# Kernel optimization log

Measured on AMD Instinct MI355X. Metric: run time of the kernel, lower is better.

Reference implementation:

```python
import jax, jax.numpy as jnp
import numpy as np

N_NODES = 50000


def _relgraphconv(x, W, Wloop, b, src, dst, etypes, n_nodes):
    # DGL RelGraphConv (regularizer=None, self_loop=True, norm=None):
    # out[i] = sum over incoming edges (j->i, rel r) of W_r @ x[j]  +  W_loop @ x[i]  +  b
    # low-mem form: transform all nodes per relation, then gather per edge.
    h_rel = jnp.einsum('ni,rio->rno', x, W)          # [R, N, out]
    msg = h_rel[etypes, src]                          # [E, out]
    agg = jax.ops.segment_sum(msg, dst, num_segments=n_nodes)  # [N, out]
    return agg + x @ Wloop + b


def setup_inputs() -> dict:
    key = jax.random.key(0)
    ks = jax.random.split(key, 12)
    N, E, n_state = N_NODES, 800000, 128
    inp = {
        'x': jax.random.normal(ks[0], (N, n_state), dtype=jnp.float32),
        'src': jax.random.randint(ks[1], (E,), 0, N, dtype=jnp.int32),
        'dst': jax.random.randint(ks[2], (E,), 0, N, dtype=jnp.int32),
        'etypes': jax.random.randint(ks[3], (E,), 0, 2, dtype=jnp.int32),
        'cell_size': jax.random.randint(ks[4], (N,), 0, 8, dtype=jnp.int32),
        'max_size': jax.random.randint(ks[5], (N,), 0, 8, dtype=jnp.int32),
        'W1': jax.random.normal(ks[6], (2, n_state, 64), dtype=jnp.float32) * 0.05,
        'loop1': jax.random.normal(ks[7], (n_state, 64), dtype=jnp.float32) * 0.05,
        'b1': jnp.zeros((64,), dtype=jnp.float32),
        'W2': jax.random.normal(ks[8], (2, 64, 64), dtype=jnp.float32) * 0.05,
        'loop2': jax.random.normal(ks[9], (64, 64), dtype=jnp.float32) * 0.05,
        'b2': jnp.zeros((64,), dtype=jnp.float32),
        'W3': jax.random.normal(ks[10], (2, 64, 2), dtype=jnp.float32) * 0.05,
        'loop3': jax.random.normal(ks[11], (64, 2), dtype=jnp.float32) * 0.05,
        'b3': jnp.zeros((2,), dtype=jnp.float32),
    }
    return inp


def reference(x, src, dst, etypes, cell_size, max_size,
              W1, loop1, b1, W2, loop2, b2, W3, loop3, b3):
    N = x.shape[0]
    h = jax.nn.relu(_relgraphconv(x, W1, loop1, b1, src, dst, etypes, N))
    h = jax.nn.relu(_relgraphconv(h, W2, loop2, b2, src, dst, etypes, N))
    h = _relgraphconv(h, W3, loop3, b3, src, dst, etypes, N)   # [N, 2]
    # action mask: col 0 = cannot upsize, col 1 = cannot downsize
    upper = cell_size >= (max_size - 1)
    lower = cell_size == 0
    mask = jnp.stack([upper, lower], axis=1)                   # [N, 2] bool
    return jnp.where(mask, h.min() - 1.0, h)
```

## Files before the change

kernel.cpp:

```cpp
#include <hip/hip_runtime.h>


#define STRIDE 64
#define BINCAP 2560

typedef unsigned short ushortT;
typedef __attribute__((ext_vector_type(8))) short short8;
typedef __attribute__((ext_vector_type(4))) float f32x4;

__device__ inline ushortT f2bf(float f) {
    union { float f; unsigned u; } v; v.f = f;
    unsigned r = v.u + 0x7FFFu + ((v.u >> 16) & 1u);
    return (ushortT)(r >> 16);
}
__device__ inline float bf2f(ushortT h) {
    union { unsigned u; float f; } v; v.u = ((unsigned)h) << 16;
    return v.f;
}

__device__ inline void atomicMinF(float* addr, float v) {
    if (v >= 0.f) atomicMin((int*)addr, __float_as_int(v));
    else          atomicMax((unsigned int*)addr, __float_as_uint(v));
}

__global__ __launch_bounds__(256) void pack_init_kernel(
    const float* __restrict__ W1, const float* __restrict__ loop1,
    const float* __restrict__ W2, const float* __restrict__ loop2,
    ushortT* __restrict__ BP1, ushortT* __restrict__ BP2,
    int* __restrict__ bincnt, float* __restrict__ minval, int NBINS) {
    int g = (int)blockIdx.x * 256 + (int)threadIdx.x;
    if (g < NBINS) bincnt[g] = 0;
    if (g == 0) *(int*)minval = 0x7f7f7f7f;
    if (g < 3072) {
        int l = g & 63, ks = (g >> 6) & 3, ct = g >> 8;
        int c = ct * 16 + (l & 15);
        int mat = c >> 6, cc = c & 63;
        int kbase = ks * 32 + (l >> 4) * 8;
        ushortT* dstp = BP1 + (size_t)g * 8;
#pragma unroll
        for (int j = 0; j < 8; ++j) {
            int k = kbase + j;
            float v = (mat < 2) ? W1[((size_t)mat * 128 + k) * 64 + cc]
                                : loop1[(size_t)k * 64 + cc];
            dstp[j] = f2bf(v);
        }
    } else {
        int s = g - 3072;
        int l = s & 63, ks = (s >> 6) & 1, ct = s >> 7;
        int c = ct * 16 + (l & 15);
        int mat = c >> 6, cc = c & 63;
        int kbase = ks * 32 + (l >> 4) * 8;
        ushortT* dstp = BP2 + (size_t)s * 8;
#pragma unroll
        for (int j = 0; j < 8; ++j) {
            int k = kbase + j;
            float v = (mat < 2) ? W2[((size_t)mat * 64 + k) * 64 + cc]
                                : loop2[(size_t)k * 64 + cc];
            dstp[j] = f2bf(v);
        }
    }
}

__global__ __launch_bounds__(256) void k1_kernel(
    const float* __restrict__ x, const ushortT* __restrict__ BP1,
    const float* __restrict__ b1,
    ushortT* __restrict__ hrelb, ushortT* __restrict__ H1b,
    const int* __restrict__ src, const int* __restrict__ dst,
    const int* __restrict__ et, int* __restrict__ bincnt, int2* __restrict__ binbuf,
    int N, int E, int NBINS, int NBA) {
    __shared__ int hist[512];
    __shared__ int gbase[512];
    __shared__ ushortT rnk[4096];

    const int t = (int)threadIdx.x;

    if ((int)blockIdx.x < NBA) {
        for (int i = t; i < NBINS; i += 256) hist[i] = 0;
        __syncthreads();
        const int base = (int)blockIdx.x * 4096;
#pragma unroll
        for (int i = 0; i < 16; ++i) {
            int e = base + t + i * 256;
            if (e < E) {
                int bb = dst[e] >> 7;
                rnk[t + i * 256] = (ushortT)atomicAdd(&hist[bb], 1);
            }
        }
        __syncthreads();
        for (int i = t; i < NBINS; i += 256) {
            int h = hist[i];
            gbase[i] = h ? atomicAdd(&bincnt[i], h) : 0;
        }
        __syncthreads();
#pragma unroll
        for (int i = 0; i < 16; ++i) {
            int e = base + t + i * 256;
            if (e < E) {
                int dd = dst[e];
                int bb = dd >> 7;
                int v = et[e] * N + src[e];
                int pos = gbase[bb] + (int)rnk[t + i * 256];
                if (pos < BINCAP)
                    binbuf[(size_t)bb * BINCAP + pos] = make_int2(dd, v);
            }
        }
        return;
    }
    const int w = t >> 6, lane = t & 63;
    const int rowbase = (((int)blockIdx.x - NBA) * 4 + w) * 16;
    const int m = lane & 15, quad = lane >> 4;
    const int nclamp = min(rowbase + m, N - 1);

    short8 a[4];
    const float* xp = x + (size_t)nclamp * 128 + quad * 8;
#pragma unroll
    for (int ks = 0; ks < 4; ++ks) {
        float4 g0 = *(const float4*)(xp + ks * 32);
        float4 g1 = *(const float4*)(xp + ks * 32 + 4);
        a[ks][0] = (short)f2bf(g0.x); a[ks][1] = (short)f2bf(g0.y);
        a[ks][2] = (short)f2bf(g0.z); a[ks][3] = (short)f2bf(g0.w);
        a[ks][4] = (short)f2bf(g1.x); a[ks][5] = (short)f2bf(g1.y);
        a[ks][6] = (short)f2bf(g1.z); a[ks][7] = (short)f2bf(g1.w);
    }

    f32x4 acc[12];
#pragma unroll
    for (int ct = 0; ct < 12; ++ct) acc[ct] = (f32x4){0.f, 0.f, 0.f, 0.f};

#pragma unroll
    for (int ks = 0; ks < 4; ++ks) {
#pragma unroll
        for (int ct = 0; ct < 12; ++ct) {
            short8 b = *(const short8*)&BP1[((size_t)(ct * 4 + ks) * 64 + lane) * 8];
            acc[ct] = __builtin_amdgcn_mfma_f32_16x16x32_bf16(a[ks], b, acc[ct], 0, 0, 0);
        }
    }

    const int node0 = rowbase + quad * 4;
#pragma unroll
    for (int ct = 0; ct < 12; ++ct) {
        int c = ct * 16 + m;
        int mat = c >> 6, cc = c & 63;
        float bias = (mat == 2) ? b1[cc] : 0.f;
#pragma unroll
        for (int j = 0; j < 4; ++j) {
            int n = node0 + j;
            if (n < N) {
                float v = acc[ct][j] + bias;
                if (mat < 2) hrelb[((size_t)mat * N + n) * 64 + cc] = f2bf(v);
                else         H1b[(size_t)n * 64 + cc] = f2bf(v);
            }
        }
    }
}

__global__ __launch_bounds__(256) void phaseB_kernel(
    const int* __restrict__ bincnt, const int2* __restrict__ binbuf,
    int* __restrict__ cnt, int* __restrict__ eidx, int N) {
    __shared__ int lcnt[128];
    const int b = (int)blockIdx.x;
    const int t = (int)threadIdx.x;
    if (t < 128) lcnt[t] = 0;
    __syncthreads();
    const int cb = min(bincnt[b], BINCAP);
    const int2* buf = binbuf + (size_t)b * BINCAP;
    for (int i = t; i < cb; i += 256) {
        int2 rec = buf[i];
        int r = atomicAdd(&lcnt[rec.x & 127], 1);
        if (r < STRIDE) eidx[(size_t)rec.x * STRIDE + r] = rec.y;
    }
    __syncthreads();
    int node = b * 128 + t;
    if (t < 128 && node < N) cnt[node] = min(lcnt[t], STRIDE);
}

__device__ __forceinline__ float gather_accum(
    const ushortT* __restrict__ hb, int my, int deg, int lane, float acc) {
    for (int j = 0; j < deg; j += 16) {
        float v[16];
#pragma unroll
        for (int q = 0; q < 16; ++q) {
            int jj = j + q;
            int sel = (jj < deg) ? jj : 0;
            int id = __shfl(my, sel, 64);
            float wgt = (jj < deg) ? 1.f : 0.f;
            v[q] = wgt * bf2f(hb[(size_t)id * 64 + lane]);
        }
        float s0 = (v[0] + v[1]) + (v[2] + v[3]);
        float s1 = (v[4] + v[5]) + (v[6] + v[7]);
        float s2 = (v[8] + v[9]) + (v[10] + v[11]);
        float s3 = (v[12] + v[13]) + (v[14] + v[15]);
        acc += (s0 + s1) + (s2 + s3);
    }
    return acc;
}

__global__ void agg1_kernel(const ushortT* __restrict__ hrelb, const int* __restrict__ eidx,
                            const int* __restrict__ cnt, ushortT* __restrict__ H1b, int N) {
    int node = (int)blockIdx.x * 4 + ((int)threadIdx.x >> 6);
    if (node >= N) return;
    int lane = (int)threadIdx.x & 63;
    int deg = cnt[node];
    int my = (lane < deg) ? eidx[(size_t)node * STRIDE + lane] : 0;
    float acc = bf2f(H1b[(size_t)node * 64 + lane]);
    acc = gather_accum(hrelb, my, deg, lane, acc);
    H1b[(size_t)node * 64 + lane] = f2bf(fmaxf(acc, 0.f));
}

__global__ __launch_bounds__(256) void gemm2_mfma(
    const ushortT* __restrict__ H1b, const ushortT* __restrict__ BP2,
    const float* __restrict__ b2,
    ushortT* __restrict__ hrel2b, ushortT* __restrict__ H2b, int N) {
    const int w = (int)threadIdx.x >> 6, lane = (int)threadIdx.x & 63;
    const int rowbase = ((int)blockIdx.x * 4 + w) * 16;
    const int m = lane & 15, quad = lane >> 4;
    const int nclamp = min(rowbase + m, N - 1);

    short8 a[2];
    const ushortT* hp = H1b + (size_t)nclamp * 64 + quad * 8;
    a[0] = *(const short8*)(hp);
    a[1] = *(const short8*)(hp + 32);

    f32x4 acc[12];
#pragma unroll
    for (int ct = 0; ct < 12; ++ct) acc[ct] = (f32x4){0.f, 0.f, 0.f, 0.f};

#pragma unroll
    for (int ks = 0; ks < 2; ++ks) {
#pragma unroll
        for (int ct = 0; ct < 12; ++ct) {
            short8 b = *(const short8*)&BP2[((size_t)(ct * 2 + ks) * 64 + lane) * 8];
            acc[ct] = __builtin_amdgcn_mfma_f32_16x16x32_bf16(a[ks], b, acc[ct], 0, 0, 0);
        }
    }

    const int node0 = rowbase + quad * 4;
#pragma unroll
    for (int ct = 0; ct < 12; ++ct) {
        int c = ct * 16 + m;
        int mat = c >> 6, cc = c & 63;
        float bias = (mat == 2) ? b2[cc] : 0.f;
#pragma unroll
        for (int j = 0; j < 4; ++j) {
            int n = node0 + j;
            if (n < N) {
                float v = acc[ct][j] + bias;
                if (mat < 2) hrel2b[((size_t)mat * N + n) * 64 + cc] = f2bf(v);
                else         H2b[(size_t)n * 64 + cc] = f2bf(v);
            }
        }
    }
}

__global__ void k3_kernel(const ushortT* __restrict__ hrel2b, const ushortT* __restrict__ H2b,
                          const int* __restrict__ eidx, const int* __restrict__ cnt,
                          const float* __restrict__ W3, const float* __restrict__ loop3,
                          const float* __restrict__ b3,
                          float* __restrict__ hrel3, float* __restrict__ H3, int N) {
    int node = (int)blockIdx.x * 4 + ((int)threadIdx.x >> 6);
    if (node >= N) return;
    int lane = (int)threadIdx.x & 63;
    int deg = cnt[node];
    int my = (lane < deg) ? eidx[(size_t)node * STRIDE + lane] : 0;
    float acc = bf2f(H2b[(size_t)node * 64 + lane]);
    acc = gather_accum(hrel2b, my, deg, lane, acc);
    float xk = fmaxf(acc, 0.f);
    float p[6];
    p[0] = xk * W3[lane * 2 + 0];
    p[1] = xk * W3[lane * 2 + 1];
    p[2] = xk * W3[(64 + lane) * 2 + 0];
    p[3] = xk * W3[(64 + lane) * 2 + 1];
    p[4] = xk * loop3[lane * 2 + 0];
    p[5] = xk * loop3[lane * 2 + 1];
#pragma unroll
    for (int mm = 32; mm >= 1; mm >>= 1) {
#pragma unroll
        for (int q = 0; q < 6; ++q) p[q] += __shfl_xor(p[q], mm, 64);
    }
    if (lane == 0) {
        hrel3[(size_t)node * 2 + 0] = p[0];
        hrel3[(size_t)node * 2 + 1] = p[1];
        hrel3[((size_t)N + node) * 2 + 0] = p[2];
        hrel3[((size_t)N + node) * 2 + 1] = p[3];
        H3[(size_t)node * 2 + 0] = p[4] + b3[0];
        H3[(size_t)node * 2 + 1] = p[5] + b3[1];
    }
}

__global__ void agg3min_kernel(const float* __restrict__ hrel3, const int* __restrict__ eidx,
                               const int* __restrict__ cnt, float* __restrict__ H3,
                               float* __restrict__ minval, int N) {
    int n = (int)blockIdx.x * 256 + (int)threadIdx.x;
    float v = 3.4e38f;
    if (n < N) {
        float a0 = H3[n * 2 + 0], a1 = H3[n * 2 + 1];
        int deg = cnt[n];
        const int* row = &eidx[(size_t)n * STRIDE];
        for (int j = 0; j < deg; j += 8) {
            float2 q[8];
            float wg[8];
#pragma unroll
            for (int qq = 0; qq < 8; ++qq) {
                int jj = j + qq;
                int sel = (jj < deg) ? jj : 0;
                int idx = row[sel];
                wg[qq] = (jj < deg) ? 1.f : 0.f;
                q[qq] = *(const float2*)&hrel3[(size_t)idx * 2];
            }
#pragma unroll
            for (int qq = 0; qq < 8; ++qq) {
                a0 += wg[qq] * q[qq].x;
                a1 += wg[qq] * q[qq].y;
            }
        }
        H3[n * 2 + 0] = a0;
        H3[n * 2 + 1] = a1;
        v = fminf(a0, a1);
    }
#pragma unroll
    for (int mm = 32; mm >= 1; mm >>= 1) v = fminf(v, __shfl_xor(v, mm, 64));
    __shared__ float s[4];
    if ((threadIdx.x & 63) == 0) s[threadIdx.x >> 6] = v;
    __syncthreads();
    if (threadIdx.x == 0)
        atomicMinF(minval, fminf(fminf(s[0], s[1]), fminf(s[2], s[3])));
}

__global__ void mask_kernel(const float* __restrict__ H3, const float* __restrict__ minval,
                            const int* __restrict__ cs, const int* __restrict__ ms,
                            float* __restrict__ out, int N) {
    int n = (int)blockIdx.x * 256 + (int)threadIdx.x;
    if (n >= N) return;
    float m = minval[0] - 1.0f;
    bool up = cs[n] >= ms[n] - 1;
    bool lo = cs[n] == 0;
    out[n * 2 + 0] = up ? m : H3[n * 2 + 0];
    out[n * 2 + 1] = lo ? m : H3[n * 2 + 1];
}

extern "C" void kernel_launch(void* const* d_in, const int* in_sizes, int n_in,
                              void* d_out, int out_size, void* d_ws, size_t ws_size,
                              hipStream_t stream) {
    const float* x     = (const float*)d_in[0];
    const int* src     = (const int*)d_in[1];
    const int* dst     = (const int*)d_in[2];
    const int* etypes  = (const int*)d_in[3];
    const int* cellsz  = (const int*)d_in[4];
    const int* maxsz   = (const int*)d_in[5];
    const float* W1    = (const float*)d_in[6];
    const float* loop1 = (const float*)d_in[7];
    const float* b1    = (const float*)d_in[8];
    const float* W2    = (const float*)d_in[9];
    const float* loop2 = (const float*)d_in[10];
    const float* b2    = (const float*)d_in[11];
    const float* W3    = (const float*)d_in[12];
    const float* loop3 = (const float*)d_in[13];
    const float* b3    = (const float*)d_in[14];
    float* out = (float*)d_out;

    const int N = in_sizes[0] / 128;
    const int E = in_sizes[1];

    char* p = (char*)d_ws;
    auto alloc = [&](size_t bytes) -> void* {
        void* r = (void*)p;
        p += ((bytes + 255) / 256) * 256;
        return r;
    };
    ushortT* hrelb  = (ushortT*)alloc((size_t)2 * N * 64 * 2);
    ushortT* H1b    = (ushortT*)alloc((size_t)N * 64 * 2);
    ushortT* hrel2b = (ushortT*)alloc((size_t)2 * N * 64 * 2);
    ushortT* H2b    = (ushortT*)alloc((size_t)N * 64 * 2);
    float* hrel3    = (float*)alloc((size_t)2 * N * 2 * 4);
    float* H3       = (float*)alloc((size_t)N * 2 * 4);
    int* cnt        = (int*)alloc((size_t)N * 4);
    int* eidx       = (int*)alloc((size_t)N * STRIDE * 4);
    ushortT* BP1    = (ushortT*)alloc((size_t)3072 * 8 * 2);
    ushortT* BP2    = (ushortT*)alloc((size_t)1536 * 8 * 2);
    float* minval   = (float*)alloc(4);

    const int NBINS = (N + 127) >> 7;
    int* bincnt     = (int*)alloc((size_t)NBINS * 4);
    int2* binbuf    = (int2*)alloc((size_t)NBINS * BINCAP * 8);
    (void)ws_size; (void)n_in; (void)out_size;

    const int NB_N   = (N + 255) / 256;
    const int NTILES = (N + 63) / 64;
    const int NB_W   = (N + 3) / 4;
    const int NBA    = (E + 4095) / 4096;

    pack_init_kernel<<<18, 256, 0, stream>>>(
        W1, loop1, W2, loop2, BP1, BP2, bincnt, minval, NBINS);

    k1_kernel<<<NBA + NTILES, 256, 0, stream>>>(
        x, BP1, b1, hrelb, H1b,
        src, dst, etypes, bincnt, binbuf, N, E, NBINS, NBA);

    phaseB_kernel<<<NBINS, 256, 0, stream>>>(bincnt, binbuf, cnt, eidx, N);

    agg1_kernel<<<NB_W, 256, 0, stream>>>(hrelb, eidx, cnt, H1b, N);

    gemm2_mfma<<<NTILES, 256, 0, stream>>>(H1b, BP2, b2, hrel2b, H2b, N);

    k3_kernel<<<NB_W, 256, 0, stream>>>(hrel2b, H2b, eidx, cnt, W3, loop3, b3,
                                        hrel3, H3, N);

    agg3min_kernel<<<NB_N, 256, 0, stream>>>(hrel3, eidx, cnt, H3, minval, N);
    mask_kernel<<<NB_N, 256, 0, stream>>>(H3, minval, cellsz, maxsz, out, N);
}
```

Measured before the change: 221.3 us.

## Aggregate before transform in layer 2 and fuse layer-3 projection into GEMM

Layer 2 now does aggregation first: per-relation sums of neighbour H1 rows are gathered into S, then one K=192 MFMA GEMM computes [S0|S1|H1]·[W2_0;W2_1;loop2]. The layer-3 projection is fused into that GEMM epilogue with shuffle reductions. This removes the separate hrel2/H2 intermediate writes and the k3 kernel, and cuts GEMM output width from 192 to 64 columns. The cost is a larger K dimension and an extra bf16 rounding of the aggregated sums before the GEMM. BP2 packing was reorganised to match the new layout.

```diff
diff --git a/kernel.cpp b/kernel.cpp
--- a/kernel.cpp
+++ b/kernel.cpp
@@ -46,16 +46,17 @@
         }
     } else {
         int s = g - 3072;
-        int l = s & 63, ks = (s >> 6) & 1, ct = s >> 7;
+        int l = s & 63;
+        int ks = (s >> 6) % 6;
+        int ct = s / 384;
         int c = ct * 16 + (l & 15);
-        int mat = c >> 6, cc = c & 63;
         int kbase = ks * 32 + (l >> 4) * 8;
         ushortT* dstp = BP2 + (size_t)s * 8;
 #pragma unroll
         for (int j = 0; j < 8; ++j) {
             int k = kbase + j;
-            float v = (mat < 2) ? W2[((size_t)mat * 64 + k) * 64 + cc]
-                                : loop2[(size_t)k * 64 + cc];
+            float v = (k < 128) ? W2[(size_t)k * 64 + c]
+                                : loop2[(size_t)(k - 128) * 64 + c];
             dstp[j] = f2bf(v);
         }
     }
@@ -207,83 +208,119 @@
     H1b[(size_t)node * 64 + lane] = f2bf(fmaxf(acc, 0.f));
 }
 
-__global__ __launch_bounds__(256) void gemm2_mfma(
-    const ushortT* __restrict__ H1b, const ushortT* __restrict__ BP2,
-    const float* __restrict__ b2,
-    ushortT* __restrict__ hrel2b, ushortT* __restrict__ H2b, int N) {
-    const int w = (int)threadIdx.x >> 6, lane = (int)threadIdx.x & 63;
-    const int rowbase = ((int)blockIdx.x * 4 + w) * 16;
-    const int m = lane & 15, quad = lane >> 4;
-    const int nclamp = min(rowbase + m, N - 1);
-
-    short8 a[2];
-    const ushortT* hp = H1b + (size_t)nclamp * 64 + quad * 8;
-    a[0] = *(const short8*)(hp);
-    a[1] = *(const short8*)(hp + 32);
-
-    f32x4 acc[12];
-#pragma unroll
-    for (int ct = 0; ct < 12; ++ct) acc[ct] = (f32x4){0.f, 0.f, 0.f, 0.f};
-
-#pragma unroll
-    for (int ks = 0; ks < 2; ++ks) {
-#pragma unroll
-        for (int ct = 0; ct < 12; ++ct) {
-            short8 b = *(const short8*)&BP2[((size_t)(ct * 2 + ks) * 64 + lane) * 8];
-            acc[ct] = __builtin_amdgcn_mfma_f32_16x16x32_bf16(a[ks], b, acc[ct], 0, 0, 0);
-        }
-    }
-
-    const int node0 = rowbase + quad * 4;
-#pragma unroll
-    for (int ct = 0; ct < 12; ++ct) {
-        int c = ct * 16 + m;
-        int mat = c >> 6, cc = c & 63;
-        float bias = (mat == 2) ? b2[cc] : 0.f;
-#pragma unroll
-        for (int j = 0; j < 4; ++j) {
-            int n = node0 + j;
-            if (n < N) {
-                float v = acc[ct][j] + bias;
-                if (mat < 2) hrel2b[((size_t)mat * N + n) * 64 + cc] = f2bf(v);
-                else         H2b[(size_t)n * 64 + cc] = f2bf(v);
-            }
-        }
-    }
-}
-
-__global__ void k3_kernel(const ushortT* __restrict__ hrel2b, const ushortT* __restrict__ H2b,
-                          const int* __restrict__ eidx, const int* __restrict__ cnt,
-                          const float* __restrict__ W3, const float* __restrict__ loop3,
-                          const float* __restrict__ b3,
-                          float* __restrict__ hrel3, float* __restrict__ H3, int N) {
+__global__ void agg2_kernel(const ushortT* __restrict__ H1b, const int* __restrict__ eidx,
+                            const int* __restrict__ cnt, ushortT* __restrict__ Sb, int N) {
     int node = (int)blockIdx.x * 4 + ((int)threadIdx.x >> 6);
     if (node >= N) return;
     int lane = (int)threadIdx.x & 63;
     int deg = cnt[node];
     int my = (lane < deg) ? eidx[(size_t)node * STRIDE + lane] : 0;
-    float acc = bf2f(H2b[(size_t)node * 64 + lane]);
-    acc = gather_accum(hrel2b, my, deg, lane, acc);
-    float xk = fmaxf(acc, 0.f);
-    float p[6];
-    p[0] = xk * W3[lane * 2 + 0];
-    p[1] = xk * W3[lane * 2 + 1];
-    p[2] = xk * W3[(64 + lane) * 2 + 0];
-    p[3] = xk * W3[(64 + lane) * 2 + 1];
-    p[4] = xk * loop3[lane * 2 + 0];
-    p[5] = xk * loop3[lane * 2 + 1];
-#pragma unroll
-    for (int mm = 32; mm >= 1; mm >>= 1) {
-#pragma unroll
-        for (int q = 0; q < 6; ++q) p[q] += __shfl_xor(p[q], mm, 64);
-    }
-    if (lane == 0) {
-        hrel3[(size_t)node * 2 + 0] = p[0];
-        hrel3[(size_t)node * 2 + 1] = p[1];
-        hrel3[((size_t)N + node) * 2 + 0] = p[2];
-        hrel3[((size_t)N + node) * 2 + 1] = p[3];
-        H3[(size_t)node * 2 + 0] = p[4] + b3[0];
-        H3[(size_t)node * 2 + 1] = p[5] + b3[1];
+    float a0 = 0.f, a1 = 0.f;
+    for (int j = 0; j < deg; j += 16) {
+        float v[16], w0[16], w1[16];
+#pragma unroll
+        for (int q = 0; q < 16; ++q) {
+            int jj = j + q;
+            int sel = (jj < deg) ? jj : 0;
+            int id = __shfl(my, sel, 64);
+            int rel = (id >= N) ? 1 : 0;
+            int row = id - rel * N;
+            float live = (jj < deg) ? 1.f : 0.f;
+            w0[q] = rel ? 0.f : live;
+            w1[q] = rel ? live : 0.f;
+            v[q] = bf2f(H1b[(size_t)row * 64 + lane]);
+        }
+#pragma unroll
+        for (int q = 0; q < 16; ++q) {
+            a0 += w0[q] * v[q];
+            a1 += w1[q] * v[q];
+        }
+    }
+    Sb[(size_t)node * 64 + lane] = f2bf(a0);
+    Sb[((size_t)N + node) * 64 + lane] = f2bf(a1);
+}
+
+__global__ __launch_bounds__(256) void gemm23_kernel(
+    const ushortT* __restrict__ Sb, const ushortT* __restrict__ H1b,
+    const ushortT* __restrict__ BP2, const float* __restrict__ b2,
+    const float* __restrict__ W3, const float* __restrict__ loop3,
+    const float* __restrict__ b3,
+    float* __restrict__ hrel3, float* __restrict__ H3, int N) {
+    const int w = (int)threadIdx.x >> 6, lane = (int)threadIdx.x & 63;
+    const int rowbase = ((int)blockIdx.x * 4 + w) * 16;
+    const int m = lane & 15, quad = lane >> 4;
+    const int nclamp = min(rowbase + m, N - 1);
+
+    f32x4 acc[4];
+#pragma unroll
+    for (int ct = 0; ct < 4; ++ct) acc[ct] = (f32x4){0.f, 0.f, 0.f, 0.f};
+
+#pragma unroll
+    for (int ks = 0; ks < 6; ++ks) {
+        const ushortT* base =
+            (ks < 2) ? (Sb + (size_t)nclamp * 64)
+          : (ks < 4) ? (Sb + ((size_t)N + nclamp) * 64)
+                     : (H1b + (size_t)nclamp * 64);
+        short8 a = *(const short8*)(base + (ks & 1) * 32 + quad * 8);
+#pragma unroll
+        for (int ct = 0; ct < 4; ++ct) {
+            short8 b = *(const short8*)&BP2[((size_t)(ct * 6 + ks) * 64 + lane) * 8];
+            acc[ct] = __builtin_amdgcn_mfma_f32_16x16x32_bf16(a, b, acc[ct], 0, 0, 0);
+        }
+    }
+
+    float h2[4][4];
+#pragma unroll
+    for (int ct = 0; ct < 4; ++ct) {
+        float bias = b2[ct * 16 + m];
+#pragma unroll
+        for (int j = 0; j < 4; ++j) h2[ct][j] = fmaxf(acc[ct][j] + bias, 0.f);
+    }
+
+    float w3v[4][6];
+#pragma unroll
+    for (int ct = 0; ct < 4; ++ct) {
+        int k = ct * 16 + m;
+        w3v[ct][0] = W3[k * 2 + 0];
+        w3v[ct][1] = W3[k * 2 + 1];
+        w3v[ct][2] = W3[(64 + k) * 2 + 0];
+        w3v[ct][3] = W3[(64 + k) * 2 + 1];
+        w3v[ct][4] = loop3[k * 2 + 0];
+        w3v[ct][5] = loop3[k * 2 + 1];
+    }
+    float p[4][6];
+#pragma unroll
+    for (int j = 0; j < 4; ++j)
+#pragma unroll
+        for (int c = 0; c < 6; ++c) p[j][c] = 0.f;
+#pragma unroll
+    for (int j = 0; j < 4; ++j)
+#pragma unroll
+        for (int ct = 0; ct < 4; ++ct)
+#pragma unroll
+            for (int c = 0; c < 6; ++c) p[j][c] += h2[ct][j] * w3v[ct][c];
+
+#pragma unroll
+    for (int mask = 1; mask <= 8; mask <<= 1) {
+#pragma unroll
+        for (int j = 0; j < 4; ++j)
+#pragma unroll
+            for (int c = 0; c < 6; ++c) p[j][c] += __shfl_xor(p[j][c], mask, 64);
+    }
+
+    if (m == 0) {
+#pragma unroll
+        for (int j = 0; j < 4; ++j) {
+            int n = rowbase + quad * 4 + j;
+            if (n < N) {
+                hrel3[(size_t)n * 2 + 0] = p[j][0];
+                hrel3[(size_t)n * 2 + 1] = p[j][1];
+                hrel3[((size_t)N + n) * 2 + 0] = p[j][2];
+                hrel3[((size_t)N + n) * 2 + 1] = p[j][3];
+                H3[(size_t)n * 2 + 0] = p[j][4] + b3[0];
+                H3[(size_t)n * 2 + 1] = p[j][5] + b3[1];
+            }
+        }
     }
 }
 
@@ -369,8 +406,7 @@
     };
     ushortT* hrelb  = (ushortT*)alloc((size_t)2 * N * 64 * 2);
     ushortT* H1b    = (ushortT*)alloc((size_t)N * 64 * 2);
-    ushortT* hrel2b = (ushortT*)alloc((size_t)2 * N * 64 * 2);
-    ushortT* H2b    = (ushortT*)alloc((size_t)N * 64 * 2);
+    ushortT* Sb     = (ushortT*)alloc((size_t)2 * N * 64 * 2);
     float* hrel3    = (float*)alloc((size_t)2 * N * 2 * 4);
     float* H3       = (float*)alloc((size_t)N * 2 * 4);
     int* cnt        = (int*)alloc((size_t)N * 4);
@@ -400,10 +436,10 @@
 
     agg1_kernel<<<NB_W, 256, 0, stream>>>(hrelb, eidx, cnt, H1b, N);
 
-    gemm2_mfma<<<NTILES, 256, 0, stream>>>(H1b, BP2, b2, hrel2b, H2b, N);
-
-    k3_kernel<<<NB_W, 256, 0, stream>>>(hrel2b, H2b, eidx, cnt, W3, loop3, b3,
-                                        hrel3, H3, N);
+    agg2_kernel<<<NB_W, 256, 0, stream>>>(H1b, eidx, cnt, Sb, N);
+
+    gemm23_kernel<<<NTILES, 256, 0, stream>>>(Sb, H1b, BP2, b2, W3, loop3, b3,
+                                              hrel3, H3, N);
 
     agg3min_kernel<<<NB_N, 256, 0, stream>>>(hrel3, eidx, cnt, H3, minval, N);
     mask_kernel<<<NB_N, 256, 0, stream>>>(H3, minval, cellsz, maxsz, out, N);
```

Result: no change. 218.6 us (-1.2%).

## Aggregate-then-transform layer 2 and fuse edge binning with weight packing and GEMM1

Applied to the files above, without the earlier changes.

Layer 2 now gathers raw H1 rows split by relation, then applies W2_r and the self-loop weight per node with scalar FMAs. This removes the separate MFMA GEMM and the hrel2/H2 intermediate buffers. Edge binning phase A is merged into the weight-pack kernel and phase B into the GEMM1 kernel, and bincnt is now zeroed with a memset, so there are fewer launches. The cost is a per-node 64x192 scalar matvec that reads weights from global memory, work that was previously done on tensor cores.

```diff
diff --git a/kernel.cpp b/kernel.cpp
--- a/kernel.cpp
+++ b/kernel.cpp
@@ -23,91 +23,108 @@
     else          atomicMax((unsigned int*)addr, __float_as_uint(v));
 }
 
-__global__ __launch_bounds__(256) void pack_init_kernel(
+__global__ __launch_bounds__(256) void pack_phaseA_kernel(
     const float* __restrict__ W1, const float* __restrict__ loop1,
     const float* __restrict__ W2, const float* __restrict__ loop2,
-    ushortT* __restrict__ BP1, ushortT* __restrict__ BP2,
-    int* __restrict__ bincnt, float* __restrict__ minval, int NBINS) {
-    int g = (int)blockIdx.x * 256 + (int)threadIdx.x;
-    if (g < NBINS) bincnt[g] = 0;
-    if (g == 0) *(int*)minval = 0x7f7f7f7f;
-    if (g < 3072) {
-        int l = g & 63, ks = (g >> 6) & 3, ct = g >> 8;
-        int c = ct * 16 + (l & 15);
-        int mat = c >> 6, cc = c & 63;
-        int kbase = ks * 32 + (l >> 4) * 8;
-        ushortT* dstp = BP1 + (size_t)g * 8;
-#pragma unroll
-        for (int j = 0; j < 8; ++j) {
-            int k = kbase + j;
-            float v = (mat < 2) ? W1[((size_t)mat * 128 + k) * 64 + cc]
-                                : loop1[(size_t)k * 64 + cc];
-            dstp[j] = f2bf(v);
-        }
-    } else {
-        int s = g - 3072;
-        int l = s & 63, ks = (s >> 6) & 1, ct = s >> 7;
-        int c = ct * 16 + (l & 15);
-        int mat = c >> 6, cc = c & 63;
-        int kbase = ks * 32 + (l >> 4) * 8;
-        ushortT* dstp = BP2 + (size_t)s * 8;
-#pragma unroll
-        for (int j = 0; j < 8; ++j) {
-            int k = kbase + j;
-            float v = (mat < 2) ? W2[((size_t)mat * 64 + k) * 64 + cc]
-                                : loop2[(size_t)k * 64 + cc];
-            dstp[j] = f2bf(v);
-        }
-    }
-}
-
-__global__ __launch_bounds__(256) void k1_kernel(
+    ushortT* __restrict__ BP1, ushortT* __restrict__ W2b,
+    float* __restrict__ minval,
+    const int* __restrict__ src, const int* __restrict__ dst,
+    const int* __restrict__ et, int* __restrict__ bincnt, int2* __restrict__ binbuf,
+    int N, int E, int NBINS) {
+    __shared__ int hist[512];
+    __shared__ int gbase[512];
+    __shared__ ushortT rnk[4096];
+    const int t = (int)threadIdx.x;
+
+    if ((int)blockIdx.x < 18) {
+        int g = (int)blockIdx.x * 256 + t;
+        if (g == 0) *(int*)minval = 0x7f7f7f7f;
+        if (g < 3072) {
+            int l = g & 63, ks = (g >> 6) & 3, ct = g >> 8;
+            int c = ct * 16 + (l & 15);
+            int mat = c >> 6, cc = c & 63;
+            int kbase = ks * 32 + (l >> 4) * 8;
+            ushortT* dstp = BP1 + (size_t)g * 8;
+#pragma unroll
+            for (int j = 0; j < 8; ++j) {
+                int k = kbase + j;
+                float v = (mat < 2) ? W1[((size_t)mat * 128 + k) * 64 + cc]
+                                    : loop1[(size_t)k * 64 + cc];
+                dstp[j] = f2bf(v);
+            }
+        } else {
+            int s = g - 3072;
+            int mat = s / 512;
+            int r8 = (s % 512) * 8;
+            ushortT* dstp = W2b + (size_t)mat * 4096 + r8;
+#pragma unroll
+            for (int j = 0; j < 8; ++j) {
+                float v = (mat < 2) ? W2[(size_t)mat * 4096 + r8 + j]
+                                    : loop2[(size_t)r8 + j];
+                dstp[j] = f2bf(v);
+            }
+        }
+        return;
+    }
+    for (int i = t; i < NBINS; i += 256) hist[i] = 0;
+    __syncthreads();
+    const int base = ((int)blockIdx.x - 18) * 4096;
+#pragma unroll
+    for (int i = 0; i < 16; ++i) {
+        int e = base + t + i * 256;
+        if (e < E) {
+            int bb = dst[e] >> 7;
+            rnk[t + i * 256] = (ushortT)atomicAdd(&hist[bb], 1);
+        }
+    }
+    __syncthreads();
+    for (int i = t; i < NBINS; i += 256) {
+        int h = hist[i];
+        gbase[i] = h ? atomicAdd(&bincnt[i], h) : 0;
+    }
+    __syncthreads();
+#pragma unroll
+    for (int i = 0; i < 16; ++i) {
+        int e = base + t + i * 256;
+        if (e < E) {
+            int dd = dst[e];
+            int bb = dd >> 7;
+            int v = et[e] * N + src[e];
+            int pos = gbase[bb] + (int)rnk[t + i * 256];
+            if (pos < BINCAP)
+                binbuf[(size_t)bb * BINCAP + pos] = make_int2(dd, v);
+        }
+    }
+}
+
+__global__ __launch_bounds__(256) void gemm1_phaseB_kernel(
     const float* __restrict__ x, const ushortT* __restrict__ BP1,
     const float* __restrict__ b1,
     ushortT* __restrict__ hrelb, ushortT* __restrict__ H1b,
-    const int* __restrict__ src, const int* __restrict__ dst,
-    const int* __restrict__ et, int* __restrict__ bincnt, int2* __restrict__ binbuf,
-    int N, int E, int NBINS, int NBA) {
-    __shared__ int hist[512];
-    __shared__ int gbase[512];
-    __shared__ ushortT rnk[4096];
-
+    const int* __restrict__ bincnt, const int2* __restrict__ binbuf,
+    int* __restrict__ cnt, int* __restrict__ eidx,
+    int N, int NBINS) {
+    __shared__ int lcnt[128];
     const int t = (int)threadIdx.x;
 
-    if ((int)blockIdx.x < NBA) {
-        for (int i = t; i < NBINS; i += 256) hist[i] = 0;
+    if ((int)blockIdx.x < NBINS) {
+        const int b = (int)blockIdx.x;
+        if (t < 128) lcnt[t] = 0;
         __syncthreads();
-        const int base = (int)blockIdx.x * 4096;
-#pragma unroll
-        for (int i = 0; i < 16; ++i) {
-            int e = base + t + i * 256;
-            if (e < E) {
-                int bb = dst[e] >> 7;
-                rnk[t + i * 256] = (ushortT)atomicAdd(&hist[bb], 1);
-            }
+        const int cb = min(bincnt[b], BINCAP);
+        const int2* buf = binbuf + (size_t)b * BINCAP;
+        for (int i = t; i < cb; i += 256) {
+            int2 rec = buf[i];
+            int r = atomicAdd(&lcnt[rec.x & 127], 1);
+            if (r < STRIDE) eidx[(size_t)rec.x * STRIDE + r] = rec.y;
         }
         __syncthreads();
-        for (int i = t; i < NBINS; i += 256) {
-            int h = hist[i];
-            gbase[i] = h ? atomicAdd(&bincnt[i], h) : 0;
-        }
-        __syncthreads();
-#pragma unroll
-        for (int i = 0; i < 16; ++i) {
-            int e = base + t + i * 256;
-            if (e < E) {
-                int dd = dst[e];
-                int bb = dd >> 7;
-                int v = et[e] * N + src[e];
-                int pos = gbase[bb] + (int)rnk[t + i * 256];
-                if (pos < BINCAP)
-                    binbuf[(size_t)bb * BINCAP + pos] = make_int2(dd, v);
-            }
-        }
+        int node = b * 128 + t;
+        if (t < 128 && node < N) cnt[node] = min(lcnt[t], STRIDE);
         return;
     }
     const int w = t >> 6, lane = t & 63;
-    const int rowbase = (((int)blockIdx.x - NBA) * 4 + w) * 16;
+    const int rowbase = (((int)blockIdx.x - NBINS) * 4 + w) * 16;
     const int m = lane & 15, quad = lane >> 4;
     const int nclamp = min(rowbase + m, N - 1);
 
@@ -152,26 +169,6 @@
             }
         }
     }
-}
-
-__global__ __launch_bounds__(256) void phaseB_kernel(
-    const int* __restrict__ bincnt, const int2* __restrict__ binbuf,
-    int* __restrict__ cnt, int* __restrict__ eidx, int N) {
-    __shared__ int lcnt[128];
-    const int b = (int)blockIdx.x;
-    const int t = (int)threadIdx.x;
-    if (t < 128) lcnt[t] = 0;
-    __syncthreads();
-    const int cb = min(bincnt[b], BINCAP);
-    const int2* buf = binbuf + (size_t)b * BINCAP;
-    for (int i = t; i < cb; i += 256) {
-        int2 rec = buf[i];
-        int r = atomicAdd(&lcnt[rec.x & 127], 1);
-        if (r < STRIDE) eidx[(size_t)rec.x * STRIDE + r] = rec.y;
-    }
-    __syncthreads();
-    int node = b * 128 + t;
-    if (t < 128 && node < N) cnt[node] = min(lcnt[t], STRIDE);
 }
 
 __device__ __forceinline__ float gather_accum(
@@ -207,71 +204,67 @@
     H1b[(size_t)node * 64 + lane] = f2bf(fmaxf(acc, 0.f));
 }
 
-__global__ __launch_bounds__(256) void gemm2_mfma(
-    const ushortT* __restrict__ H1b, const ushortT* __restrict__ BP2,
-    const float* __restrict__ b2,
-    ushortT* __restrict__ hrel2b, ushortT* __restrict__ H2b, int N) {
-    const int w = (int)threadIdx.x >> 6, lane = (int)threadIdx.x & 63;
-    const int rowbase = ((int)blockIdx.x * 4 + w) * 16;
-    const int m = lane & 15, quad = lane >> 4;
-    const int nclamp = min(rowbase + m, N - 1);
-
-    short8 a[2];
-    const ushortT* hp = H1b + (size_t)nclamp * 64 + quad * 8;
-    a[0] = *(const short8*)(hp);
-    a[1] = *(const short8*)(hp + 32);
-
-    f32x4 acc[12];
-#pragma unroll
-    for (int ct = 0; ct < 12; ++ct) acc[ct] = (f32x4){0.f, 0.f, 0.f, 0.f};
-
-#pragma unroll
-    for (int ks = 0; ks < 2; ++ks) {
-#pragma unroll
-        for (int ct = 0; ct < 12; ++ct) {
-            short8 b = *(const short8*)&BP2[((size_t)(ct * 2 + ks) * 64 + lane) * 8];
-            acc[ct] = __builtin_amdgcn_mfma_f32_16x16x32_bf16(a[ks], b, acc[ct], 0, 0, 0);
-        }
-    }
-
-    const int node0 = rowbase + quad * 4;
-#pragma unroll
-    for (int ct = 0; ct < 12; ++ct) {
-        int c = ct * 16 + m;
-        int mat = c >> 6, cc = c & 63;
-        float bias = (mat == 2) ? b2[cc] : 0.f;
-#pragma unroll
-        for (int j = 0; j < 4; ++j) {
-            int n = node0 + j;
-            if (n < N) {
-                float v = acc[ct][j] + bias;
-                if (mat < 2) hrel2b[((size_t)mat * N + n) * 64 + cc] = f2bf(v);
-                else         H2b[(size_t)n * 64 + cc] = f2bf(v);
-            }
-        }
-    }
-}
-
-__global__ void k3_kernel(const ushortT* __restrict__ hrel2b, const ushortT* __restrict__ H2b,
-                          const int* __restrict__ eidx, const int* __restrict__ cnt,
-                          const float* __restrict__ W3, const float* __restrict__ loop3,
-                          const float* __restrict__ b3,
-                          float* __restrict__ hrel3, float* __restrict__ H3, int N) {
+__global__ void agg2c_kernel(const ushortT* __restrict__ H1b, const int* __restrict__ eidx,
+                             const int* __restrict__ cnt, const ushortT* __restrict__ W2b,
+                             const float* __restrict__ b2,
+                             const float* __restrict__ W3, const float* __restrict__ loop3,
+                             const float* __restrict__ b3,
+                             float* __restrict__ hrel3, float* __restrict__ H3, int N) {
     int node = (int)blockIdx.x * 4 + ((int)threadIdx.x >> 6);
     if (node >= N) return;
     int lane = (int)threadIdx.x & 63;
     int deg = cnt[node];
     int my = (lane < deg) ? eidx[(size_t)node * STRIDE + lane] : 0;
-    float acc = bf2f(H2b[(size_t)node * 64 + lane]);
-    acc = gather_accum(hrel2b, my, deg, lane, acc);
-    float xk = fmaxf(acc, 0.f);
+    float h1self = bf2f(H1b[(size_t)node * 64 + lane]);
+
+    float a0 = 0.f, a1 = 0.f;
+    for (int j = 0; j < deg; j += 16) {
+        float v[16], w0[16], w1[16];
+#pragma unroll
+        for (int q = 0; q < 16; ++q) {
+            int jj = j + q;
+            int sel = (jj < deg) ? jj : 0;
+            int id = __shfl(my, sel, 64);
+            int rel = (id >= N) ? 1 : 0;
+            int row = id - rel * N;
+            float live = (jj < deg) ? 1.f : 0.f;
+            w0[q] = rel ? 0.f : live;
+            w1[q] = rel ? live : 0.f;
+            v[q] = bf2f(H1b[(size_t)row * 64 + lane]);
+        }
+#pragma unroll
+        for (int q = 0; q < 16; ++q) {
+            a0 += w0[q] * v[q];
+            a1 += w1[q] * v[q];
+        }
+    }
+
+    float acc = b2[lane];
+    for (int k = 0; k < 64; k += 8) {
+        float s0[8], s1[8], hh[8];
+#pragma unroll
+        for (int q = 0; q < 8; ++q) {
+            s0[q] = __shfl(a0, k + q, 64);
+            s1[q] = __shfl(a1, k + q, 64);
+            hh[q] = __shfl(h1self, k + q, 64);
+        }
+#pragma unroll
+        for (int q = 0; q < 8; ++q) {
+            float w0 = bf2f(W2b[(size_t)(k + q) * 64 + lane]);
+            float w1 = bf2f(W2b[4096 + (size_t)(k + q) * 64 + lane]);
+            float wl = bf2f(W2b[8192 + (size_t)(k + q) * 64 + lane]);
+            acc += s0[q] * w0 + s1[q] * w1 + hh[q] * wl;
+        }
+    }
+    float h2 = fmaxf(acc, 0.f);
+
     float p[6];
-    p[0] = xk * W3[lane * 2 + 0];
-    p[1] = xk * W3[lane * 2 + 1];
-    p[2] = xk * W3[(64 + lane) * 2 + 0];
-    p[3] = xk * W3[(64 + lane) * 2 + 1];
-    p[4] = xk * loop3[lane * 2 + 0];
-    p[5] = xk * loop3[lane * 2 + 1];
+    p[0] = h2 * W3[lane * 2 + 0];
+    p[1] = h2 * W3[lane * 2 + 1];
+    p[2] = h2 * W3[(64 + lane) * 2 + 0];
+    p[3] = h2 * W3[(64 + lane) * 2 + 1];
+    p[4] = h2 * loop3[lane * 2 + 0];
+    p[5] = h2 * loop3[lane * 2 + 1];
 #pragma unroll
     for (int mm = 32; mm >= 1; mm >>= 1) {
 #pragma unroll
@@ -369,14 +362,12 @@
     };
     ushortT* hrelb  = (ushortT*)alloc((size_t)2 * N * 64 * 2);
     ushortT* H1b    = (ushortT*)alloc((size_t)N * 64 * 2);
-    ushortT* hrel2b = (ushortT*)alloc((size_t)2 * N * 64 * 2);
-    ushortT* H2b    = (ushortT*)alloc((size_t)N * 64 * 2);
     float* hrel3    = (float*)alloc((size_t)2 * N * 2 * 4);
     float* H3       = (float*)alloc((size_t)N * 2 * 4);
     int* cnt        = (int*)alloc((size_t)N * 4);
     int* eidx       = (int*)alloc((size_t)N * STRIDE * 4);
     ushortT* BP1    = (ushortT*)alloc((size_t)3072 * 8 * 2);
-    ushortT* BP2    = (ushortT*)alloc((size_t)1536 * 8 * 2);
+    ushortT* W2b    = (ushortT*)alloc((size_t)3 * 4096 * 2);
     float* minval   = (float*)alloc(4);
 
     const int NBINS = (N + 127) >> 7;
@@ -389,22 +380,21 @@
     const int NB_W   = (N + 3) / 4;
     const int NBA    = (E + 4095) / 4096;
 
-    pack_init_kernel<<<18, 256, 0, stream>>>(
-        W1, loop1, W2, loop2, BP1, BP2, bincnt, minval, NBINS);
-
-    k1_kernel<<<NBA + NTILES, 256, 0, stream>>>(
-        x, BP1, b1, hrelb, H1b,
-        src, dst, etypes, bincnt, binbuf, N, E, NBINS, NBA);
-
-    phaseB_kernel<<<NBINS, 256, 0, stream>>>(bincnt, binbuf, cnt, eidx, N);
+    hipMemsetAsync(bincnt, 0, (size_t)NBINS * 4, stream);
+
+    pack_phaseA_kernel<<<18 + NBA, 256, 0, stream>>>(
+        W1, loop1, W2, loop2, BP1, W2b, minval,
+        src, dst, etypes, bincnt, binbuf, N, E, NBINS);
+
+    gemm1_phaseB_kernel<<<NBINS + NTILES, 256, 0, stream>>>(
+        x, BP1, b1, hrelb, H1b, bincnt, binbuf, cnt, eidx, N, NBINS);
 
     agg1_kernel<<<NB_W, 256, 0, stream>>>(hrelb, eidx, cnt, H1b, N);
 
-    gemm2_mfma<<<NTILES, 256, 0, stream>>>(H1b, BP2, b2, hrel2b, H2b, N);
-
-    k3_kernel<<<NB_W, 256, 0, stream>>>(hrel2b, H2b, eidx, cnt, W3, loop3, b3,
-                                        hrel3, H3, N);
+    agg2c_kernel<<<NB_W, 256, 0, stream>>>(H1b, eidx, cnt, W2b, b2,
+                                           W3, loop3, b3, hrel3, H3, N);
 
     agg3min_kernel<<<NB_N, 256, 0, stream>>>(hrel3, eidx, cnt, H3, minval, N);
+
     mask_kernel<<<NB_N, 256, 0, stream>>>(H3, minval, cellsz, maxsz, out, N);
 }
```

Measured after the change: 313.8 us. 1.42x slower.
